# Kernel optimization log

Measured on AMD Instinct MI355X. Metric: run time of the kernel, lower is better.

Reference implementation:

```python
import jax, jax.numpy as jnp
import numpy as np

N = 50000        # nodes
E = 800000       # edges (avg degree 16)
F = 64           # NUM_NODE_FEATURES == NUM_FILTERS
P = 32           # allocation.NUM_PHYS (policy logits per graph)
G = 64           # graphs in batch
MAX_DEG = 10     # PyG MFConv default max_degree


def setup_inputs() -> dict:
    key = jax.random.key(0)
    ks = jax.random.split(key, 12)
    x = jax.random.normal(ks[0], (N, F), jnp.float32)
    edge_index = jax.random.randint(ks[1], (2, E), 0, N, dtype=jnp.int32)
    batch = jnp.sort(jax.random.randint(ks[2], (N,), 0, G, dtype=jnp.int32))
    s = 1.0 / np.sqrt(F)
    return {
        "x": x,
        "edge_index": edge_index,
        "batch": batch,
        # GCNConv conv_in: F -> F
        "W_in": jax.random.normal(ks[3], (F, F), jnp.float32) * s,
        "b_in": jnp.zeros((F,), jnp.float32),
        # GCNConv conv_1: F -> F
        "W1": jax.random.normal(ks[4], (F, F), jnp.float32) * s,
        "b1": jnp.zeros((F,), jnp.float32),
        # MFConv conv_val: F -> 1, per-degree weights (deg 0..MAX_DEG)
        "Wl_val": jax.random.normal(ks[5], (MAX_DEG + 1, F, 1), jnp.float32) * s,
        "bl_val": jnp.zeros((MAX_DEG + 1, 1), jnp.float32),
        "Wr_val": jax.random.normal(ks[6], (MAX_DEG + 1, F, 1), jnp.float32) * s,
        # GCNConv conv_policy: F -> P
        "W_pol": jax.random.normal(ks[7], (F, P), jnp.float32) * s,
        "b_pol": jnp.zeros((P,), jnp.float32),
    }


def gcn_conv(x, edge_index, W, b):
    # PyG GCNConv: add self-loops, symmetric normalization, linear, scatter-add.
    src, dst = edge_index[0], edge_index[1]
    loop = jnp.arange(N, dtype=src.dtype)
    src = jnp.concatenate([src, loop])
    dst = jnp.concatenate([dst, loop])
    deg = jax.ops.segment_sum(jnp.ones_like(dst, x.dtype), dst, num_segments=N)
    dinv = jnp.where(deg > 0, jax.lax.rsqrt(deg), 0.0)
    norm = dinv[src] * dinv[dst]                 # [E+N]
    h = x @ W                                    # [N, out]
    out = jax.ops.segment_sum(norm[:, None] * h[src], dst, num_segments=N)
    return out + b


def mf_conv(x, edge_index, Wl, bl, Wr):
    # PyG MFConv: sum-aggregate neighbors, per-degree linear transforms.
    src, dst = edge_index[0], edge_index[1]
    h = jax.ops.segment_sum(x[src], dst, num_segments=N)     # neighbor sum [N,F]
    deg = jax.ops.segment_sum(jnp.ones((src.shape[0],), jnp.int32), dst, num_segments=N)
    deg = jnp.clip(deg, 0, MAX_DEG)                          # [N]
    # out = lins_l[deg](h) + lins_r[deg](x)  (lins_r has no bias)
    out = (jnp.einsum("nf,nfo->no", h, Wl[deg]) + bl[deg]
           + jnp.einsum("nf,nfo->no", x, Wr[deg]))
    return out


def reference(x, edge_index, batch, W_in, b_in, W1, b1, Wl_val, bl_val, Wr_val, W_pol, b_pol):
    h = gcn_conv(x, edge_index, W_in, b_in)
    h = gcn_conv(h, edge_index, W1, b1)
    val = mf_conv(h, edge_index, Wl_val, bl_val, Wr_val)          # [N,1]
    val = jax.ops.segment_sum(val, batch, num_segments=G)         # global_add_pool [G,1]
    pol = gcn_conv(h, edge_index, W_pol, b_pol)                   # [N,P]
    pol_sum = jax.ops.segment_sum(pol, batch, num_segments=G)
    cnt = jax.ops.segment_sum(jnp.ones((N,), x.dtype), batch, num_segments=G)
    pol = pol_sum / jnp.maximum(cnt, 1.0)[:, None]                # global_mean_pool [G,P]
    return (pol, val)
```

## Files before the change

### kernel.cpp

```cpp
#include <hip/hip_runtime.h>

#define F 64
#define P 32
#define MAXD 10
#define NGRP 8

__device__ __forceinline__ unsigned short f2bf(float f) {
  unsigned b = __float_as_uint(f);
  return (unsigned short)((b + 0x7FFFu + ((b >> 16) & 1u)) >> 16);
}
__device__ __forceinline__ unsigned pk2(float a, float b) {
  return (unsigned)f2bf(a) | ((unsigned)f2bf(b) << 16);
}
__device__ __forceinline__ float blo(unsigned u) { return __uint_as_float(u << 16); }
__device__ __forceinline__ float bhi(unsigned u) { return __uint_as_float(u & 0xFFFF0000u); }

__global__ void k_zero(float4* __restrict__ p, int n4) {
  int i = blockIdx.x * blockDim.x + threadIdx.x;
  int stride = gridDim.x * blockDim.x;
  float4 z = make_float4(0.f, 0.f, 0.f, 0.f);
  for (int idx = i; idx < n4; idx += stride) p[idx] = z;
}

__global__ void k_count_deg(const int* __restrict__ dst, int* __restrict__ deg, int E, int N) {
  int r = blockIdx.x & (NGRP - 1);
  float scale = (float)NGRP / (float)N;
  int gblk = blockIdx.x >> 3;
  int i = gblk * blockDim.x + threadIdx.x;
  int stride = (gridDim.x >> 3) * blockDim.x;
  int E4 = E >> 2;
  const int4* d4p = (const int4*)dst;
  for (int e4 = i; e4 < E4; e4 += stride) {
    int4 d4 = d4p[e4];
    int rr;
    rr = min(NGRP - 1, (int)((float)d4.x * scale)); if (rr == r) atomicAdd(&deg[d4.x], 1);
    rr = min(NGRP - 1, (int)((float)d4.y * scale)); if (rr == r) atomicAdd(&deg[d4.y], 1);
    rr = min(NGRP - 1, (int)((float)d4.z * scale)); if (rr == r) atomicAdd(&deg[d4.z], 1);
    rr = min(NGRP - 1, (int)((float)d4.w * scale)); if (rr == r) atomicAdd(&deg[d4.w], 1);
  }
  for (int e = (E & ~3) + i; e < E; e += stride) {
    int d = dst[e];
    int rr = min(NGRP - 1, (int)((float)d * scale));
    if (rr == r) atomicAdd(&deg[d], 1);
  }
}

__global__ void k_bsum(const int* __restrict__ deg, int* __restrict__ bsum, int N) {
  __shared__ int s[256];
  int t = threadIdx.x;
  int n = blockIdx.x * 256 + t;
  s[t] = (n < N) ? deg[n] : 0;
  __syncthreads();
  for (int o = 128; o > 0; o >>= 1) {
    if (t < o) s[t] += s[t + o];
    __syncthreads();
  }
  if (t == 0) bsum[blockIdx.x] = s[0];
}

__global__ void k_scan_fin(const int* __restrict__ deg, const int* __restrict__ bsum,
                           int* __restrict__ off, int* __restrict__ cur,
                           float* __restrict__ dinv, int N, int NB) {
  __shared__ int sb[256];
  __shared__ int s[256];
  int t = threadIdx.x;
  int b = blockIdx.x;
  sb[t] = (t < NB && t < b) ? bsum[t] : 0;
  __syncthreads();
  for (int o = 128; o > 0; o >>= 1) {
    if (t < o) sb[t] += sb[t + o];
    __syncthreads();
  }
  int base = sb[0];
  int n = b * 256 + t;
  int v = (n < N) ? deg[n] : 0;
  s[t] = v;
  __syncthreads();
  for (int o = 1; o < 256; o <<= 1) {
    int u = (t >= o) ? s[t - o] : 0;
    __syncthreads();
    s[t] += u;
    __syncthreads();
  }
  if (n < N) {
    int ex = base + s[t] - v;
    off[n] = ex;
    cur[n] = ex;
    dinv[n] = rsqrtf((float)(v + 1));
    if (n == N - 1) off[N] = ex + v;
  }
}

__global__ void k_fill(const int* __restrict__ src, const int* __restrict__ dst,
                       int* __restrict__ cur, int* __restrict__ csr, int E, int N) {
  int r = blockIdx.x & (NGRP - 1);
  float scale = (float)NGRP / (float)N;
  int gblk = blockIdx.x >> 3;
  int i = gblk * blockDim.x + threadIdx.x;
  int stride = (gridDim.x >> 3) * blockDim.x;
  int E4 = E >> 2;
  const int4* d4p = (const int4*)dst;
  for (int e4 = i; e4 < E4; e4 += stride) {
    int4 d4 = d4p[e4];
    int e = e4 * 4;
    int rr;
    rr = min(NGRP - 1, (int)((float)d4.x * scale));
    if (rr == r) { int pos = atomicAdd(&cur[d4.x], 1); csr[pos] = src[e]; }
    rr = min(NGRP - 1, (int)((float)d4.y * scale));
    if (rr == r) { int pos = atomicAdd(&cur[d4.y], 1); csr[pos] = src[e + 1]; }
    rr = min(NGRP - 1, (int)((float)d4.z * scale));
    if (rr == r) { int pos = atomicAdd(&cur[d4.z], 1); csr[pos] = src[e + 2]; }
    rr = min(NGRP - 1, (int)((float)d4.w * scale));
    if (rr == r) { int pos = atomicAdd(&cur[d4.w], 1); csr[pos] = src[e + 3]; }
  }
  for (int e = (E & ~3) + i; e < E; e += stride) {
    int d = dst[e];
    int rr = min(NGRP - 1, (int)((float)d * scale));
    if (rr == r) { int pos = atomicAdd(&cur[d], 1); csr[pos] = src[e]; }
  }
}

__global__ void k_scale16(const float* __restrict__ x, const float* __restrict__ dinv,
                          uint2* __restrict__ xs, int N) {
  int i = blockIdx.x * blockDim.x + threadIdx.x;
  int stride = gridDim.x * blockDim.x;
  int tot = N * (F / 4);
  const float4* x4 = (const float4*)x;
  for (int idx = i; idx < tot; idx += stride) {
    int n = idx >> 4;
    float d = dinv[n];
    float4 v = x4[idx];
    uint2 p;
    p.x = pk2(v.x * d, v.y * d);
    p.y = pk2(v.z * d, v.w * d);
    xs[idx] = p;
  }
}

__device__ __forceinline__ float rdlane(float v, int srclane) {
  return __int_as_float(__builtin_amdgcn_readlane(__float_as_int(v), srclane));
}

__device__ __forceinline__ void addbf(float4& a, uint2 p) {
  a.x += blo(p.x); a.y += bhi(p.x); a.z += blo(p.y); a.w += bhi(p.y);
}

template <bool WRITE_SCALED>
__global__ void k_gcn(const unsigned* __restrict__ xs, const int* __restrict__ csr,
                      const int* __restrict__ off, const float* __restrict__ dinv,
                      const float* __restrict__ W, const float* __restrict__ bias,
                      unsigned short* __restrict__ out, int N) {
  int wid = (blockIdx.x * blockDim.x + threadIdx.x) >> 6;
  int lane = threadIdx.x & 63;
  int nwaves = (gridDim.x * blockDim.x) >> 6;
  int g = lane >> 4, l = lane & 15;
  float w[F];
#pragma unroll
  for (int k = 0; k < F; ++k) w[k] = W[k * F + lane];
  float bv = bias[lane];
  for (int base = wid * 4; base < N; base += nwaves * 4) {
    int n = min(base + g, N - 1);
    int e0 = off[n], e1 = off[n + 1];
    float dnode = dinv[n];
    float4 acc = make_float4(0.f, 0.f, 0.f, 0.f);
    addbf(acc, *(const uint2*)&xs[(size_t)n * 32 + l * 2]);
    for (int win = e0; win < e1; win += 16) {
      int m = min(16, e1 - win);
      int ce = (win + l < e1) ? csr[win + l] : 0;
      int j = 0;
      for (; j + 8 <= m; j += 8) {
        int s0 = __shfl(ce, g * 16 + j + 0, 64);
        int s1 = __shfl(ce, g * 16 + j + 1, 64);
        int s2 = __shfl(ce, g * 16 + j + 2, 64);
        int s3 = __shfl(ce, g * 16 + j + 3, 64);
        int s4 = __shfl(ce, g * 16 + j + 4, 64);
        int s5 = __shfl(ce, g * 16 + j + 5, 64);
        int s6 = __shfl(ce, g * 16 + j + 6, 64);
        int s7 = __shfl(ce, g * 16 + j + 7, 64);
        uint2 q0 = *(const uint2*)&xs[(size_t)s0 * 32 + l * 2];
        uint2 q1 = *(const uint2*)&xs[(size_t)s1 * 32 + l * 2];
        uint2 q2 = *(const uint2*)&xs[(size_t)s2 * 32 + l * 2];
        uint2 q3 = *(const uint2*)&xs[(size_t)s3 * 32 + l * 2];
        uint2 q4 = *(const uint2*)&xs[(size_t)s4 * 32 + l * 2];
        uint2 q5 = *(const uint2*)&xs[(size_t)s5 * 32 + l * 2];
        uint2 q6 = *(const uint2*)&xs[(size_t)s6 * 32 + l * 2];
        uint2 q7 = *(const uint2*)&xs[(size_t)s7 * 32 + l * 2];
        addbf(acc, q0); addbf(acc, q1); addbf(acc, q2); addbf(acc, q3);
        addbf(acc, q4); addbf(acc, q5); addbf(acc, q6); addbf(acc, q7);
      }
      for (; j + 4 <= m; j += 4) {
        int s0 = __shfl(ce, g * 16 + j + 0, 64);
        int s1 = __shfl(ce, g * 16 + j + 1, 64);
        int s2 = __shfl(ce, g * 16 + j + 2, 64);
        int s3 = __shfl(ce, g * 16 + j + 3, 64);
        uint2 q0 = *(const uint2*)&xs[(size_t)s0 * 32 + l * 2];
        uint2 q1 = *(const uint2*)&xs[(size_t)s1 * 32 + l * 2];
        uint2 q2 = *(const uint2*)&xs[(size_t)s2 * 32 + l * 2];
        uint2 q3 = *(const uint2*)&xs[(size_t)s3 * 32 + l * 2];
        addbf(acc, q0); addbf(acc, q1); addbf(acc, q2); addbf(acc, q3);
      }
      for (; j < m; ++j) {
        int s = __shfl(ce, g * 16 + j, 64);
        addbf(acc, *(const uint2*)&xs[(size_t)s * 32 + l * 2]);
      }
    }
#pragma unroll
    for (int gg = 0; gg < 4; ++gg) {
      float y0 = 0.f, y1 = 0.f, y2 = 0.f, y3 = 0.f;
#pragma unroll
      for (int k = 0; k < F; k += 4) {
        y0 += rdlane(acc.x, gg * 16 + (k >> 2)) * w[k + 0];
        y1 += rdlane(acc.y, gg * 16 + (k >> 2)) * w[k + 1];
        y2 += rdlane(acc.z, gg * 16 + (k >> 2)) * w[k + 2];
        y3 += rdlane(acc.w, gg * 16 + (k >> 2)) * w[k + 3];
      }
      float dd = rdlane(dnode, gg * 16);
      float y = dd * ((y0 + y1) + (y2 + y3)) + bv;
      if (WRITE_SCALED) y *= dd;
      int nn = base + gg;
      if (nn < N) out[(size_t)nn * F + lane] = f2bf(y);
    }
  }
}

__global__ void k_mfpol(const unsigned* __restrict__ H, const int* __restrict__ csr,
                        const int* __restrict__ off, const float* __restrict__ dinv,
                        const float* __restrict__ Wl, const float* __restrict__ bl,
                        const float* __restrict__ Wr, const int* __restrict__ batch,
                        float* __restrict__ Uacc, float* __restrict__ valg,
                        float* __restrict__ cntg, int N, int G) {
  __shared__ float Ua[2][64];
  __shared__ float va[2], ca[2];
  int t = threadIdx.x;
  if (t < 128) Ua[t >> 6][t & 63] = 0.f;
  if (t < 2) { va[t] = 0.f; ca[t] = 0.f; }
  __syncthreads();
  int base16 = blockIdx.x * 16;
  int gmin = batch[base16];
  int lane = t & 63;
  int g = lane >> 4, l = lane & 15;
  int ni = (t >> 6) * 4 + g;
  bool valid = (base16 + ni) < N;
  int n = valid ? base16 + ni : N - 1;
  int e0 = off[n], e1 = off[n + 1];
  float dn = dinv[n];
  float4 ah = make_float4(0.f, 0.f, 0.f, 0.f);
  float4 aw = make_float4(0.f, 0.f, 0.f, 0.f);
  for (int win = e0; win < e1; win += 16) {
    int m = min(16, e1 - win);
    bool p = (win + l < e1);
    int ce = p ? csr[win + l] : 0;
    float cd = p ? dinv[ce] : 0.f;
    int j = 0;
    for (; j + 8 <= m; j += 8) {
      int s0 = __shfl(ce, g * 16 + j + 0, 64);
      int s1 = __shfl(ce, g * 16 + j + 1, 64);
      int s2 = __shfl(ce, g * 16 + j + 2, 64);
      int s3 = __shfl(ce, g * 16 + j + 3, 64);
      int s4 = __shfl(ce, g * 16 + j + 4, 64);
      int s5 = __shfl(ce, g * 16 + j + 5, 64);
      int s6 = __shfl(ce, g * 16 + j + 6, 64);
      int s7 = __shfl(ce, g * 16 + j + 7, 64);
      float d0 = __shfl(cd, g * 16 + j + 0, 64);
      float d1 = __shfl(cd, g * 16 + j + 1, 64);
      float d2 = __shfl(cd, g * 16 + j + 2, 64);
      float d3 = __shfl(cd, g * 16 + j + 3, 64);
      float d4 = __shfl(cd, g * 16 + j + 4, 64);
      float d5 = __shfl(cd, g * 16 + j + 5, 64);
      float d6 = __shfl(cd, g * 16 + j + 6, 64);
      float d7 = __shfl(cd, g * 16 + j + 7, 64);
      uint2 q0 = *(const uint2*)&H[(size_t)s0 * 32 + l * 2];
      uint2 q1 = *(const uint2*)&H[(size_t)s1 * 32 + l * 2];
      uint2 q2 = *(const uint2*)&H[(size_t)s2 * 32 + l * 2];
      uint2 q3 = *(const uint2*)&H[(size_t)s3 * 32 + l * 2];
      uint2 q4 = *(const uint2*)&H[(size_t)s4 * 32 + l * 2];
      uint2 q5 = *(const uint2*)&H[(size_t)s5 * 32 + l * 2];
      uint2 q6 = *(const uint2*)&H[(size_t)s6 * 32 + l * 2];
      uint2 q7 = *(const uint2*)&H[(size_t)s7 * 32 + l * 2];
      float fx, fy, fz, fw;
      fx = blo(q0.x); fy = bhi(q0.x); fz = blo(q0.y); fw = bhi(q0.y);
      ah.x += fx; ah.y += fy; ah.z += fz; ah.w += fw;
      aw.x += d0 * fx; aw.y += d0 * fy; aw.z += d0 * fz; aw.w += d0 * fw;
      fx = blo(q1.x); fy = bhi(q1.x); fz = blo(q1.y); fw = bhi(q1.y);
      ah.x += fx; ah.y += fy; ah.z += fz; ah.w += fw;
      aw.x += d1 * fx; aw.y += d1 * fy; aw.z += d1 * fz; aw.w += d1 * fw;
      fx = blo(q2.x); fy = bhi(q2.x); fz = blo(q2.y); fw = bhi(q2.y);
      ah.x += fx; ah.y += fy; ah.z += fz; ah.w += fw;
      aw.x += d2 * fx; aw.y += d2 * fy; aw.z += d2 * fz; aw.w += d2 * fw;
      fx = blo(q3.x); fy = bhi(q3.x); fz = blo(q3.y); fw = bhi(q3.y);
      ah.x += fx; ah.y += fy; ah.z += fz; ah.w += fw;
      aw.x += d3 * fx; aw.y += d3 * fy; aw.z += d3 * fz; aw.w += d3 * fw;
      fx = blo(q4.x); fy = bhi(q4.x); fz = blo(q4.y); fw = bhi(q4.y);
      ah.x += fx; ah.y += fy; ah.z += fz; ah.w += fw;
      aw.x += d4 * fx; aw.y += d4 * fy; aw.z += d4 * fz; aw.w += d4 * fw;
      fx = blo(q5.x); fy = bhi(q5.x); fz = blo(q5.y); fw = bhi(q5.y);
      ah.x += fx; ah.y += fy; ah.z += fz; ah.w += fw;
      aw.x += d5 * fx; aw.y += d5 * fy; aw.z += d5 * fz; aw.w += d5 * fw;
      fx = blo(q6.x); fy = bhi(q6.x); fz = blo(q6.y); fw = bhi(q6.y);
      ah.x += fx; ah.y += fy; ah.z += fz; ah.w += fw;
      aw.x += d6 * fx; aw.y += d6 * fy; aw.z += d6 * fz; aw.w += d6 * fw;
      fx = blo(q7.x); fy = bhi(q7.x); fz = blo(q7.y); fw = bhi(q7.y);
      ah.x += fx; ah.y += fy; ah.z += fz; ah.w += fw;
      aw.x += d7 * fx; aw.y += d7 * fy; aw.z += d7 * fz; aw.w += d7 * fw;
    }
    for (; j < m; ++j) {
      int s = __shfl(ce, g * 16 + j, 64);
      float dd = __shfl(cd, g * 16 + j, 64);
      uint2 q = *(const uint2*)&H[(size_t)s * 32 + l * 2];
      float fx = blo(q.x), fy = bhi(q.x), fz = blo(q.y), fw = bhi(q.y);
      ah.x += fx; ah.y += fy; ah.z += fz; ah.w += fw;
      aw.x += dd * fx; aw.y += dd * fy; aw.z += dd * fz; aw.w += dd * fw;
    }
  }
  int dc = min(e1 - e0, MAXD);
  uint2 qn = *(const uint2*)&H[(size_t)n * 32 + l * 2];
  float4 hn = make_float4(blo(qn.x), bhi(qn.x), blo(qn.y), bhi(qn.y));
  float4 wl4 = *(const float4*)&Wl[dc * F + l * 4];
  float4 wr4 = *(const float4*)&Wr[dc * F + l * 4];
  float part = ah.x * wl4.x + ah.y * wl4.y + ah.z * wl4.z + ah.w * wl4.w
             + hn.x * wr4.x + hn.y * wr4.y + hn.z * wr4.z + hn.w * wr4.w;
#pragma unroll
  for (int o = 1; o < 16; o <<= 1) part += __shfl_xor(part, o, 64);
  float vout = part + bl[dc];
  float4 r;
  r.x = (aw.x + dn * hn.x) * dn;
  r.y = (aw.y + dn * hn.y) * dn;
  r.z = (aw.z + dn * hn.z) * dn;
  r.w = (aw.w + dn * hn.w) * dn;
  if (valid) {
    int bg = batch[n];
    int slot = bg - gmin;
    if (slot < 2) {
      atomicAdd(&Ua[slot][l * 4 + 0], r.x);
      atomicAdd(&Ua[slot][l * 4 + 1], r.y);
      atomicAdd(&Ua[slot][l * 4 + 2], r.z);
      atomicAdd(&Ua[slot][l * 4 + 3], r.w);
      if (l == 0) { atomicAdd(&va[slot], vout); atomicAdd(&ca[slot], 1.f); }
    } else {
      atomicAdd(&Uacc[bg * F + l * 4 + 0], r.x);
      atomicAdd(&Uacc[bg * F + l * 4 + 1], r.y);
      atomicAdd(&Uacc[bg * F + l * 4 + 2], r.z);
      atomicAdd(&Uacc[bg * F + l * 4 + 3], r.w);
      if (l == 0) { atomicAdd(&valg[bg], vout); atomicAdd(&cntg[bg], 1.f); }
    }
  }
  __syncthreads();
  if (t < 128) {
    int slot = t >> 6, f = t & 63;
    int bg = gmin + slot;
    if (bg < G) {
      atomicAdd(&Uacc[bg * F + f], Ua[slot][f]);
      if (f == 0) { atomicAdd(&valg[bg], va[slot]); atomicAdd(&cntg[bg], ca[slot]); }
    }
  }
}

__global__ void k_polfin(const float* __restrict__ Uacc, const float* __restrict__ valg,
                         const float* __restrict__ cntg, const float* __restrict__ W_pol,
                         const float* __restrict__ b_pol, float* __restrict__ out, int G) {
  int i = blockIdx.x * blockDim.x + threadIdx.x;
  if (i < G * P) {
    int g = i >> 5, p = i & 31;
    float s = 0.f;
#pragma unroll
    for (int k = 0; k < F; ++k) s += Uacc[g * F + k] * W_pol[k * P + p];
    out[i] = s / fmaxf(cntg[g], 1.f) + b_pol[p];
  }
  if (i < G) out[(size_t)G * P + i] = valg[i];
}

extern "C" void kernel_launch(void* const* d_in, const int* in_sizes, int n_in,
                              void* d_out, int out_size, void* d_ws, size_t ws_size,
                              hipStream_t stream) {
  const float* x = (const float*)d_in[0];
  const int* ei = (const int*)d_in[1];
  const int* batch = (const int*)d_in[2];
  const float* W_in = (const float*)d_in[3];
  const float* b_in = (const float*)d_in[4];
  const float* W1 = (const float*)d_in[5];
  const float* b1 = (const float*)d_in[6];
  const float* Wl = (const float*)d_in[7];
  const float* bl = (const float*)d_in[8];
  const float* Wr = (const float*)d_in[9];
  const float* W_pol = (const float*)d_in[10];
  const float* b_pol = (const float*)d_in[11];
  float* out = (float*)d_out;

  const int N = in_sizes[0] / F;
  const int E = in_sizes[1] / 2;
  const int G = out_size / (P + 1);
  const int* esrc = ei;
  const int* edst = ei + E;
  const int NB = (N + 255) / 256;

  char* ws = (char*)d_ws;
  size_t o = 0;
  auto alloc = [&](size_t bytes) {
    char* r = ws + o;
    o = (o + bytes + 255) & ~(size_t)255;
    return r;
  };
  char* zbase = ws;
  int* deg = (int*)alloc((size_t)N * 4);
  float* Uacc = (float*)alloc((size_t)G * F * 4);
  float* valg = (float*)alloc((size_t)G * 4);
  float* cntg = (float*)alloc((size_t)G * 4);
  size_t zbytes = o;
  int* off = (int*)alloc((size_t)(N + 1) * 4);
  int* cur = (int*)alloc((size_t)N * 4);
  float* dinv = (float*)alloc((size_t)N * 4);
  int* csr = (int*)alloc((size_t)E * 4);
  int* bsum = (int*)alloc(1024 * 4);
  unsigned* xs16 = (unsigned*)alloc((size_t)N * F * 2);
  unsigned* t16 = (unsigned*)alloc((size_t)N * F * 2);
  unsigned* h16 = (unsigned*)alloc((size_t)N * F * 2);
  (void)ws_size; (void)n_in;

  const int bs = 256;
  int zn4 = (int)(zbytes / 16);
  k_zero<<<(zn4 + bs - 1) / bs, bs, 0, stream>>>((float4*)zbase, zn4);

  k_count_deg<<<2048, bs, 0, stream>>>(edst, deg, E, N);
  k_bsum<<<NB, bs, 0, stream>>>(deg, bsum, N);
  k_scan_fin<<<NB, bs, 0, stream>>>(deg, bsum, off, cur, dinv, N, NB);
  k_fill<<<2048, bs, 0, stream>>>(esrc, edst, cur, csr, E, N);

  k_scale16<<<2048, bs, 0, stream>>>(x, dinv, (uint2*)xs16, N);

  k_gcn<true><<<1024, bs, 0, stream>>>(xs16, csr, off, dinv, W_in, b_in,
                                       (unsigned short*)t16, N);
  k_gcn<false><<<1024, bs, 0, stream>>>(t16, csr, off, dinv, W1, b1,
                                        (unsigned short*)h16, N);

  int mfBlocks = (N + 15) / 16;
  k_mfpol<<<mfBlocks, bs, 0, stream>>>(h16, csr, off, dinv, Wl, bl, Wr, batch,
                                       Uacc, valg, cntg, N, G);

  k_polfin<<<(G * P + bs - 1) / bs, bs, 0, stream>>>(Uacc, valg, cntg, W_pol, b_pol, out, G);
}
```

Before: 222.1 us.

## Simplify degree counting, shrink mfpol unroll, and double GCN grid size

The degree-count kernel drops its 8-way destination-range partitioning, where each block group atomically updated only one slice of nodes, and now does plain atomics on every edge with half the blocks. This removes the redundant 8x reads of dst but gives up the atomic locality the partitioning provided. The value/policy aggregation loop is unrolled by 4 instead of 8, with tree-style sums to shorten dependency chains and reduce register pressure. The GCN kernels are launched with twice as many blocks.

```diff
diff --git a/kernel.cpp b/kernel.cpp
--- a/kernel.cpp
+++ b/kernel.cpp
@@ -22,27 +22,19 @@
   for (int idx = i; idx < n4; idx += stride) p[idx] = z;
 }
 
-__global__ void k_count_deg(const int* __restrict__ dst, int* __restrict__ deg, int E, int N) {
-  int r = blockIdx.x & (NGRP - 1);
-  float scale = (float)NGRP / (float)N;
-  int gblk = blockIdx.x >> 3;
-  int i = gblk * blockDim.x + threadIdx.x;
-  int stride = (gridDim.x >> 3) * blockDim.x;
+__global__ void k_count_deg(const int* __restrict__ dst, int* __restrict__ deg, int E) {
+  int i = blockIdx.x * blockDim.x + threadIdx.x;
+  int stride = gridDim.x * blockDim.x;
   int E4 = E >> 2;
   const int4* d4p = (const int4*)dst;
   for (int e4 = i; e4 < E4; e4 += stride) {
-    int4 d4 = d4p[e4];
-    int rr;
-    rr = min(NGRP - 1, (int)((float)d4.x * scale)); if (rr == r) atomicAdd(&deg[d4.x], 1);
-    rr = min(NGRP - 1, (int)((float)d4.y * scale)); if (rr == r) atomicAdd(&deg[d4.y], 1);
-    rr = min(NGRP - 1, (int)((float)d4.z * scale)); if (rr == r) atomicAdd(&deg[d4.z], 1);
-    rr = min(NGRP - 1, (int)((float)d4.w * scale)); if (rr == r) atomicAdd(&deg[d4.w], 1);
-  }
-  for (int e = (E & ~3) + i; e < E; e += stride) {
-    int d = dst[e];
-    int rr = min(NGRP - 1, (int)((float)d * scale));
-    if (rr == r) atomicAdd(&deg[d], 1);
-  }
+    int4 d = d4p[e4];
+    atomicAdd(&deg[d.x], 1);
+    atomicAdd(&deg[d.y], 1);
+    atomicAdd(&deg[d.z], 1);
+    atomicAdd(&deg[d.w], 1);
+  }
+  for (int e = (E & ~3) + i; e < E; e += stride) atomicAdd(&deg[dst[e]], 1);
 }
 
 __global__ void k_bsum(const int* __restrict__ deg, int* __restrict__ bsum, int N) {
@@ -252,56 +244,31 @@
     int ce = p ? csr[win + l] : 0;
     float cd = p ? dinv[ce] : 0.f;
     int j = 0;
-    for (; j + 8 <= m; j += 8) {
+    for (; j + 4 <= m; j += 4) {
       int s0 = __shfl(ce, g * 16 + j + 0, 64);
       int s1 = __shfl(ce, g * 16 + j + 1, 64);
       int s2 = __shfl(ce, g * 16 + j + 2, 64);
       int s3 = __shfl(ce, g * 16 + j + 3, 64);
-      int s4 = __shfl(ce, g * 16 + j + 4, 64);
-      int s5 = __shfl(ce, g * 16 + j + 5, 64);
-      int s6 = __shfl(ce, g * 16 + j + 6, 64);
-      int s7 = __shfl(ce, g * 16 + j + 7, 64);
       float d0 = __shfl(cd, g * 16 + j + 0, 64);
       float d1 = __shfl(cd, g * 16 + j + 1, 64);
       float d2 = __shfl(cd, g * 16 + j + 2, 64);
       float d3 = __shfl(cd, g * 16 + j + 3, 64);
-      float d4 = __shfl(cd, g * 16 + j + 4, 64);
-      float d5 = __shfl(cd, g * 16 + j + 5, 64);
-      float d6 = __shfl(cd, g * 16 + j + 6, 64);
-      float d7 = __shfl(cd, g * 16 + j + 7, 64);
       uint2 q0 = *(const uint2*)&H[(size_t)s0 * 32 + l * 2];
       uint2 q1 = *(const uint2*)&H[(size_t)s1 * 32 + l * 2];
       uint2 q2 = *(const uint2*)&H[(size_t)s2 * 32 + l * 2];
       uint2 q3 = *(const uint2*)&H[(size_t)s3 * 32 + l * 2];
-      uint2 q4 = *(const uint2*)&H[(size_t)s4 * 32 + l * 2];
-      uint2 q5 = *(const uint2*)&H[(size_t)s5 * 32 + l * 2];
-      uint2 q6 = *(const uint2*)&H[(size_t)s6 * 32 + l * 2];
-      uint2 q7 = *(const uint2*)&H[(size_t)s7 * 32 + l * 2];
-      float fx, fy, fz, fw;
-      fx = blo(q0.x); fy = bhi(q0.x); fz = blo(q0.y); fw = bhi(q0.y);
-      ah.x += fx; ah.y += fy; ah.z += fz; ah.w += fw;
-      aw.x += d0 * fx; aw.y += d0 * fy; aw.z += d0 * fz; aw.w += d0 * fw;
-      fx = blo(q1.x); fy = bhi(q1.x); fz = blo(q1.y); fw = bhi(q1.y);
-      ah.x += fx; ah.y += fy; ah.z += fz; ah.w += fw;
-      aw.x += d1 * fx; aw.y += d1 * fy; aw.z += d1 * fz; aw.w += d1 * fw;
-      fx = blo(q2.x); fy = bhi(q2.x); fz = blo(q2.y); fw = bhi(q2.y);
-      ah.x += fx; ah.y += fy; ah.z += fz; ah.w += fw;
-      aw.x += d2 * fx; aw.y += d2 * fy; aw.z += d2 * fz; aw.w += d2 * fw;
-      fx = blo(q3.x); fy = bhi(q3.x); fz = blo(q3.y); fw = bhi(q3.y);
-      ah.x += fx; ah.y += fy; ah.z += fz; ah.w += fw;
-      aw.x += d3 * fx; aw.y += d3 * fy; aw.z += d3 * fz; aw.w += d3 * fw;
-      fx = blo(q4.x); fy = bhi(q4.x); fz = blo(q4.y); fw = bhi(q4.y);
-      ah.x += fx; ah.y += fy; ah.z += fz; ah.w += fw;
-      aw.x += d4 * fx; aw.y += d4 * fy; aw.z += d4 * fz; aw.w += d4 * fw;
-      fx = blo(q5.x); fy = bhi(q5.x); fz = blo(q5.y); fw = bhi(q5.y);
-      ah.x += fx; ah.y += fy; ah.z += fz; ah.w += fw;
-      aw.x += d5 * fx; aw.y += d5 * fy; aw.z += d5 * fz; aw.w += d5 * fw;
-      fx = blo(q6.x); fy = bhi(q6.x); fz = blo(q6.y); fw = bhi(q6.y);
-      ah.x += fx; ah.y += fy; ah.z += fz; ah.w += fw;
-      aw.x += d6 * fx; aw.y += d6 * fy; aw.z += d6 * fz; aw.w += d6 * fw;
-      fx = blo(q7.x); fy = bhi(q7.x); fz = blo(q7.y); fw = bhi(q7.y);
-      ah.x += fx; ah.y += fy; ah.z += fz; ah.w += fw;
-      aw.x += d7 * fx; aw.y += d7 * fy; aw.z += d7 * fz; aw.w += d7 * fw;
+      float f0x = blo(q0.x), f0y = bhi(q0.x), f0z = blo(q0.y), f0w = bhi(q0.y);
+      float f1x = blo(q1.x), f1y = bhi(q1.x), f1z = blo(q1.y), f1w = bhi(q1.y);
+      float f2x = blo(q2.x), f2y = bhi(q2.x), f2z = blo(q2.y), f2w = bhi(q2.y);
+      float f3x = blo(q3.x), f3y = bhi(q3.x), f3z = blo(q3.y), f3w = bhi(q3.y);
+      ah.x += (f0x + f1x) + (f2x + f3x);
+      ah.y += (f0y + f1y) + (f2y + f3y);
+      ah.z += (f0z + f1z) + (f2z + f3z);
+      ah.w += (f0w + f1w) + (f2w + f3w);
+      aw.x += (d0 * f0x + d1 * f1x) + (d2 * f2x + d3 * f3x);
+      aw.y += (d0 * f0y + d1 * f1y) + (d2 * f2y + d3 * f3y);
+      aw.z += (d0 * f0z + d1 * f1z) + (d2 * f2z + d3 * f3z);
+      aw.w += (d0 * f0w + d1 * f1w) + (d2 * f2w + d3 * f3w);
     }
     for (; j < m; ++j) {
       int s = __shfl(ce, g * 16 + j, 64);
@@ -420,16 +387,16 @@
   int zn4 = (int)(zbytes / 16);
   k_zero<<<(zn4 + bs - 1) / bs, bs, 0, stream>>>((float4*)zbase, zn4);
 
-  k_count_deg<<<2048, bs, 0, stream>>>(edst, deg, E, N);
+  k_count_deg<<<1024, bs, 0, stream>>>(edst, deg, E);
   k_bsum<<<NB, bs, 0, stream>>>(deg, bsum, N);
   k_scan_fin<<<NB, bs, 0, stream>>>(deg, bsum, off, cur, dinv, N, NB);
   k_fill<<<2048, bs, 0, stream>>>(esrc, edst, cur, csr, E, N);
 
   k_scale16<<<2048, bs, 0, stream>>>(x, dinv, (uint2*)xs16, N);
 
-  k_gcn<true><<<1024, bs, 0, stream>>>(xs16, csr, off, dinv, W_in, b_in,
+  k_gcn<true><<<2048, bs, 0, stream>>>(xs16, csr, off, dinv, W_in, b_in,
                                        (unsigned short*)t16, N);
-  k_gcn<false><<<1024, bs, 0, stream>>>(t16, csr, off, dinv, W1, b1,
+  k_gcn<false><<<2048, bs, 0, stream>>>(t16, csr, off, dinv, W1, b1,
                                         (unsigned short*)h16, N);
 
   int mfBlocks = (N + 15) / 16;
```

Result: no change. 220.9 us (-0.5%).
